# Optimization experiments

Measured on AMD Instinct MI355X. Metric: run time of the kernel, lower is better.

The kernel has to match this reference:

```python
import jax, jax.numpy as jnp
import numpy as np

LSTM = 400   # lstm_size
M = 20       # output_mixture_components
K = 10       # attention_mixture_components
A = 73       # alphabet_size


def setup_inputs() -> dict:
    key = jax.random.key(0)
    ks = jax.random.split(key, 24)
    B, T, U = 128, 800, 64

    def p(k, shape, scale=0.05):
        return jax.random.normal(k, shape, dtype=jnp.float32) * scale

    in1 = 3 + A                 # lstm1 input: [window, x]
    in2 = 3 + LSTM + A          # lstm2 input: [x, h1, window]
    in3 = 3 + 2 * LSTM + A      # lstm3 input: [x, h1, h2, window]

    inp = {
        "inputs": jax.random.normal(ks[0], (B, T, 3), dtype=jnp.float32) * 0.1,
        "char_seq": jax.random.randint(ks[1], (B, U), 0, A),
        "char_seq_lengths": jax.random.randint(ks[2], (B,), U // 2, U + 1),
        "bias": jnp.full((B,), 0.5, dtype=jnp.float32),
        # LSTMCell params (torch layout: gates order i,f,g,o)
        "Wih1": p(ks[3], (4 * LSTM, in1)), "Whh1": p(ks[4], (4 * LSTM, LSTM)),
        "bih1": p(ks[5], (4 * LSTM,)),    "bhh1": p(ks[6], (4 * LSTM,)),
        "Wih2": p(ks[7], (4 * LSTM, in2)), "Whh2": p(ks[8], (4 * LSTM, LSTM)),
        "bih2": p(ks[9], (4 * LSTM,)),    "bhh2": p(ks[10], (4 * LSTM,)),
        "Wih3": p(ks[11], (4 * LSTM, in3)), "Whh3": p(ks[12], (4 * LSTM, LSTM)),
        "bih3": p(ks[13], (4 * LSTM,)),    "bhh3": p(ks[14], (4 * LSTM,)),
        # Attention: h1 -> (alpha_hat, beta_hat, kappa_hat), 3K outputs
        "Wa": p(ks[15], (3 * K, LSTM)), "ba": p(ks[16], (3 * K,)),
        # GMM head: [h1,h2,h3] -> 6M+1 params
        "Wg": p(ks[17], (6 * M + 1, 3 * LSTM)), "bg": p(ks[18], (6 * M + 1,)),
    }
    return inp


def _lstm_cell(x, h, c, Wih, Whh, bih, bhh):
    gates = x @ Wih.T + bih + h @ Whh.T + bhh
    i, f, g, o = jnp.split(gates, 4, axis=-1)
    c = jax.nn.sigmoid(f) * c + jax.nn.sigmoid(i) * jnp.tanh(g)
    h = jax.nn.sigmoid(o) * jnp.tanh(c)
    return h, c


def reference(inputs, char_seq, char_seq_lengths, bias,
              Wih1, Whh1, bih1, bhh1,
              Wih2, Whh2, bih2, bhh2,
              Wih3, Whh3, bih3, bhh3,
              Wa, ba, Wg, bg):
    B, T, _ = inputs.shape
    U = char_seq.shape[1]
    oh = jax.nn.one_hot(char_seq, A, dtype=jnp.float32)            # [B,U,A]
    u = jnp.arange(U, dtype=jnp.float32)                            # [U]
    umask = (u[None, :] < char_seq_lengths[:, None].astype(jnp.float32)).astype(jnp.float32)
    bias_c = bias[:, None]

    def step(carry, x_t):
        h1, c1, h2, c2, h3, c3, window, kappa = carry
        h1, c1 = _lstm_cell(jnp.concatenate([window, x_t], 1), h1, c1, Wih1, Whh1, bih1, bhh1)
        # Gaussian-mixture attention window (Graves 2013)
        ap = h1 @ Wa.T + ba                                         # [B,3K]
        alpha_h, beta_h, kappa_h = jnp.split(ap, 3, axis=1)
        alpha = jnp.exp(alpha_h)
        beta = jnp.exp(beta_h)
        kappa = kappa + jnp.exp(kappa_h)                            # [B,K]
        # phi[b,u] = sum_k alpha exp(-beta (kappa-u)^2)
        g = jnp.exp(-beta[:, :, None] * (kappa[:, :, None] - u) ** 2)  # [B,K,U]
        phi = jnp.einsum('bk,bku->bu', alpha, g) * umask
        window = jnp.einsum('bu,bua->ba', phi, oh)                  # [B,A]
        h2, c2 = _lstm_cell(jnp.concatenate([x_t, h1, window], 1), h2, c2, Wih2, Whh2, bih2, bhh2)
        h3, c3 = _lstm_cell(jnp.concatenate([x_t, h1, h2, window], 1), h3, c3, Wih3, Whh3, bih3, bhh3)
        # GMM output layer with sampling bias
        out = jnp.concatenate([h1, h2, h3], 1) @ Wg.T + bg          # [B,6M+1]
        pi_hat = out[:, :M]
        mus = out[:, M:3 * M]
        sig_hat = out[:, 3 * M:5 * M]
        rho_hat = out[:, 5 * M:6 * M]
        e_hat = out[:, 6 * M:]
        pis = jax.nn.softmax(pi_hat * (1.0 + bias_c), axis=-1)
        sigmas = jnp.exp(sig_hat - bias_c)
        rhos = jnp.tanh(rho_hat)
        es = jax.nn.sigmoid(e_hat)
        return (h1, c1, h2, c2, h3, c3, window, kappa), (pis, sigmas, rhos, mus, es)

    z = lambda d: jnp.zeros((B, d), dtype=jnp.float32)
    carry0 = (z(LSTM), z(LSTM), z(LSTM), z(LSTM), z(LSTM), z(LSTM), z(A), z(K))
    _, outs = jax.lax.scan(step, carry0, jnp.swapaxes(inputs, 0, 1))
    pis, sigmas, rhos, mus, es = (jnp.swapaxes(o, 0, 1) for o in outs)  # [B,T,*]
    return pis, sigmas, rhos, mus, es
```

## Files before the change

### kernel.cpp

```cpp
#include <hip/hip_runtime.h>
#include <stdint.h>

typedef short s8v __attribute__((ext_vector_type(8)));
typedef _Float16 h8v __attribute__((ext_vector_type(8)));
typedef float f4v __attribute__((ext_vector_type(4)));
typedef unsigned short u16;
typedef unsigned int u32;
typedef unsigned long long u64;

#define TT 800
#define BB 128
#define UU 64
#define ALP 73
#define DD 400

#define G_BATCH 32
#define N_CLUS 4
#define N_MEM 50
#define NTHREADS 256

#define CX0 0
#define CX1 32
#define CWIN 64
#define CWINLO 160
#define CH1 256
#define CH2 672
#define CH3 1088
#define ACT_STRIDE 3072

#define NC1 17
#define NC2 30
#define NC3 43
#define NCO 39
#define NCA 13
#define F1 5
#define F2 8
#define F3 11
#define FA 4
#define FO 10

#define ACT_BYTES (32*ACT_STRIDE)
#define H1LO_OFF ACT_BYTES
#define H1LO_STRIDE 896
#define RBUF_OFF (H1LO_OFF + 32*H1LO_STRIDE)
#define ABK_OFF (RBUF_OFF + 16384)
#define WINS_OFF (ABK_OFF + 3840)
#define CHAR_OFF (RBUF_OFF + 32768)
#define LENS_OFF (CHAR_OFF + 2048)
#define BIASC_OFF (LENS_OFF + 128)
#define BCI_OFF (BIASC_OFF + 128)
#define BAS_OFF (BCI_OFF + 384)
#define BGS_OFF (BAS_OFF + 128)
#define LDS_TOTAL (BGS_OFF + 128)

#define OFF_SIG ((size_t)BB*TT*20)
#define OFF_RHO ((size_t)BB*TT*60)
#define OFF_MU  ((size_t)BB*TT*80)
#define OFF_ES  ((size_t)BB*TT*120)

#define HBUF_U32 25600

#define MFMA16(A,B,C) __builtin_amdgcn_mfma_f32_16x16x32_f16(__builtin_bit_cast(h8v,(A)),__builtin_bit_cast(h8v,(B)),(C),0,0,0)

#define AST(p,v) __hip_atomic_store((p),(v),__ATOMIC_RELAXED,__HIP_MEMORY_SCOPE_AGENT)
#define ALD(p)   __hip_atomic_load((p),__ATOMIC_RELAXED,__HIP_MEMORY_SCOPE_AGENT)

__device__ __forceinline__ u16 f16b(float x) {
  _Float16 h = (_Float16)x;
  return __builtin_bit_cast(u16, h);
}
__device__ __forceinline__ float f2f(u16 h) {
  return (float)__builtin_bit_cast(_Float16, h);
}
__device__ __forceinline__ float sigm(float x) { return 1.f / (1.f + __expf(-x)); }
__device__ __forceinline__ float tanhe(float x) {
  float e = __expf(-2.f * fabsf(x));
  float r = (1.f - e) / (1.f + e);
  return (x < 0.f) ? -r : r;
}
__device__ __forceinline__ int imin(int a, int b) { return a < b ? a : b; }
__device__ __forceinline__ int lstm_row(int mem, int n, int r) {
  return (n*2 + (r>>3))*400 + mem*8 + (r&7);
}
__device__ __forceinline__ int out_orow(int rc) {
  if (rc < 20) return rc;
  if (rc < 60) return 60 + (rc-20);
  if (rc < 80) return 100 + (rc-60);
  if (rc < 120) return 20 + (rc-80);
  if (rc == 120) return 120;
  return -1;
}
__device__ __forceinline__ s8v gath(const float* W, int ld, int grow, int cb, int valid, int k0) {
  union { s8v v; u16 u[8]; } r;
  #pragma unroll
  for (int j = 0; j < 8; ++j) {
    int k = k0 + j;
    float x = 0.f;
    if (grow >= 0 && k < valid) x = W[(size_t)grow * ld + cb + k];
    r.u[j] = f16b(x);
  }
  return r.v;
}
__device__ __forceinline__ s8v gathlo(const float* W, int ld, int grow, int cb, int valid, int k0) {
  union { s8v v; u16 u[8]; } r;
  #pragma unroll
  for (int j = 0; j < 8; ++j) {
    int k = k0 + j;
    float x = 0.f;
    if (grow >= 0 && k < valid) x = W[(size_t)grow * ld + cb + k];
    u16 hi = f16b(x);
    r.u[j] = f16b(x - f2f(hi));
  }
  return r.v;
}

extern "C" __global__ __launch_bounds__(NTHREADS, 1)
void hwrnn(const float* __restrict__ xin, const int* __restrict__ chq,
           const int* __restrict__ lenq, const float* __restrict__ biasq,
           const float* __restrict__ Wih1, const float* __restrict__ Whh1,
           const float* __restrict__ bih1, const float* __restrict__ bhh1,
           const float* __restrict__ Wih2, const float* __restrict__ Whh2,
           const float* __restrict__ bih2, const float* __restrict__ bhh2,
           const float* __restrict__ Wih3, const float* __restrict__ Whh3,
           const float* __restrict__ bih3, const float* __restrict__ bhh3,
           const float* __restrict__ Wa, const float* __restrict__ ba,
           const float* __restrict__ Wg, const float* __restrict__ bg,
           float* __restrict__ dout, u32* __restrict__ barr,
           u32* __restrict__ h1ring, u32* __restrict__ h2g, u32* __restrict__ h3g,
           u32* __restrict__ h1glo)
{
  extern __shared__ __align__(16) char sm[];
  const int tid = threadIdx.x;
  const int wv = tid >> 6;
  const int ln = tid & 63;
  const int cl = blockIdx.x & 3;
  const int mem = blockIdx.x >> 2;
  const int B0 = cl * G_BATCH;

  const int arow = ln & 15;
  const int k0 = (ln >> 4) * 8;
  const int ahi = (ln >> 4) * 16;
  const int axor = (ln & 7) << 4;
  const int rb0 = arow * ACT_STRIDE;
  const int rb1 = (16 + arow) * ACT_STRIDE;
  const int hb0 = H1LO_OFF + arow * H1LO_STRIDE;
  const int hb1 = H1LO_OFF + (16 + arow) * H1LO_STRIDE;
  const f4v az = {0.f, 0.f, 0.f, 0.f};

  for (int i = tid; i * 16 < RBUF_OFF; i += NTHREADS) *(f4v*)(sm + i*16) = az;
  for (int i = tid; i < 32*UU; i += NTHREADS) {
    int b = i >> 6, u = i & 63;
    ((unsigned char*)(sm + CHAR_OFF))[i] = (unsigned char)chq[(B0 + b)*UU + u];
  }
  if (tid < 32) {
    ((int*)(sm + LENS_OFF))[tid] = lenq[B0 + tid];
    ((float*)(sm + BIASC_OFF))[tid] = biasq[B0 + tid];
    ((float*)(sm + BAS_OFF))[tid] = (tid < 30) ? ba[tid] : 0.f;
    float v = 0.f;
    if (mem == 0) { int orow = out_orow(tid); if (orow >= 0) v = bg[orow]; }
    else if (mem >= 1 && mem <= 6 && tid < 16) {
      int orow = out_orow((mem+1)*16 + tid); if (orow >= 0) v = bg[orow];
    }
    ((float*)(sm + BGS_OFF))[tid] = v;
  }
  if (tid < 96) {
    int l = tid >> 5, r = tid & 31;
    int grow = lstm_row(mem, r >> 4, r & 15);
    const float* bi = (l == 0) ? bih1 : (l == 1) ? bih2 : bih3;
    const float* bh = (l == 0) ? bhh1 : (l == 1) ? bhh2 : bhh3;
    ((float*)(sm + BCI_OFF))[l*32 + r] = bi[grow] + bh[grow];
  }

  s8v wf1[F1][2], wf2[F2][2], wf3[F3][2], wfa[FA][2], walo[FA][2], wfo[2][FO];
  #pragma unroll
  for (int i = 0; i < F1; ++i) {
    int c = wv + 4*i;
    #pragma unroll
    for (int n = 0; n < 2; ++n) {
      s8v v = {0,0,0,0,0,0,0,0};
      if (c < NC1) {
        int grow = lstm_row(mem, n, arow);
        if (c == 0)      v = gath(Wih1, 76, grow, 73, 3, k0);
        else if (c <= 3) v = gath(Wih1, 76, grow, (c-1)*32, imin(32, 73-(c-1)*32), k0);
        else             v = gath(Whh1, 400, grow, (c-4)*32, imin(32, 400-(c-4)*32), k0);
      }
      wf1[i][n] = v;
    }
  }
  #pragma unroll
  for (int i = 0; i < F2; ++i) {
    int c = wv + 4*i;
    #pragma unroll
    for (int n = 0; n < 2; ++n) {
      s8v v = {0,0,0,0,0,0,0,0};
      if (c < NC2) {
        int grow = lstm_row(mem, n, arow);
        if (c == 0)       v = gath(Wih2, 476, grow, 0, 3, k0);
        else if (c <= 13) v = gath(Wih2, 476, grow, 3+32*(c-1), imin(32, 400-32*(c-1)), k0);
        else if (c <= 16) v = gath(Wih2, 476, grow, 403+32*(c-14), imin(32, 73-32*(c-14)), k0);
        else              v = gath(Whh2, 400, grow, 32*(c-17), imin(32, 400-32*(c-17)), k0);
      }
      wf2[i][n] = v;
    }
  }
  #pragma unroll
  for (int i = 0; i < F3; ++i) {
    int c = wv + 4*i;
    #pragma unroll
    for (int n = 0; n < 2; ++n) {
      s8v v = {0,0,0,0,0,0,0,0};
      if (c < NC3) {
        int grow = lstm_row(mem, n, arow);
        if (c == 0)       v = gath(Wih3, 876, grow, 0, 3, k0);
        else if (c <= 13) v = gath(Wih3, 876, grow, 3+32*(c-1), imin(32, 400-32*(c-1)), k0);
        else if (c <= 26) v = gath(Wih3, 876, grow, 403+32*(c-14), imin(32, 400-32*(c-14)), k0);
        else if (c <= 29) v = gath(Wih3, 876, grow, 803+32*(c-27), imin(32, 73-32*(c-27)), k0);
        else              v = gath(Whh3, 400, grow, 32*(c-30), imin(32, 400-32*(c-30)), k0);
      }
      wf3[i][n] = v;
    }
  }
  #pragma unroll
  for (int i = 0; i < FA; ++i) {
    int c = wv + 4*i;
    #pragma unroll
    for (int n = 0; n < 2; ++n) {
      s8v v = {0,0,0,0,0,0,0,0}, vl = v;
      if (c < NCA) {
        int rr = n*16 + arow;
        int grow = (rr < 30) ? rr : -1;
        v  = gath  (Wa, 400, grow, 32*c, imin(32, 400-32*c), k0);
        vl = gathlo(Wa, 400, grow, 32*c, imin(32, 400-32*c), k0);
      }
      wfa[i][n] = v; walo[i][n] = vl;
    }
  }
  #pragma unroll
  for (int o = 0; o < 2; ++o) {
    #pragma unroll
    for (int i = 0; i < FO; ++i) {
      s8v v = {0,0,0,0,0,0,0,0};
      int c = wv + 4*i;
      bool have = (mem == 0) || (mem >= 1 && mem <= 6 && o == 0);
      if (have && c < NCO) {
        int ct = (mem == 0) ? o : (mem + 1);
        int grow = out_orow(ct*16 + arow);
        if (c <= 12)      v = gath(Wg, 1200, grow, 32*c, imin(32, 400-32*c), k0);
        else if (c <= 25) v = gath(Wg, 1200, grow, 400+32*(c-13), imin(32, 400-32*(c-13)), k0);
        else              v = gath(Wg, 1200, grow, 800+32*(c-26), imin(32, 400-32*(c-26)), k0);
      }
      wfo[o][i] = v;
    }
  }

  auto LDA0 = [&](int cb2) -> s8v { return *(const s8v*)(sm + rb0 + ((cb2 + ahi) ^ axor)); };
  auto LDA1 = [&](int cb2) -> s8v { return *(const s8v*)(sm + rb1 + ((cb2 + ahi) ^ axor)); };
  auto LDL0 = [&](int cb2) -> s8v { return *(const s8v*)(sm + hb0 + ((cb2 + ahi) ^ axor)); };
  auto LDL1 = [&](int cb2) -> s8v { return *(const s8v*)(sm + hb1 + ((cb2 + ahi) ^ axor)); };
  auto WPART = [&](int slot, f4v a) {
    *(f4v*)(sm + RBUF_OFF + (((slot*4 + wv)*256) + (ln & 15)*16 + (ln >> 4)*4)*4) = a;
  };
  auto RBF = [&](int slot, int w, int col, int row) -> float {
    return ((float*)(sm + RBUF_OFF))[(slot*4 + w)*256 + col*16 + row];
  };
  auto RLD = [&](const u32* ring, int half) -> s8v {
    union { s8v v; u64 q[2]; } r;
    r.q[0] = ALD((const u64*)ring + ((size_t)(B0 + arow + 16*half)*DD + k0 >> 2));
    r.q[1] = ALD((const u64*)ring + ((size_t)(B0 + arow + 16*half)*DD + k0 + 4 >> 2));
    return r.v;
  };
  const int ub = tid >> 3, uu = tid & 7;
  auto LUPD = [&](int sb, int l, float& c, u32* hg, u32* hlo) {
    int mt = ub >> 4, rw = ub & 15;
    const float* bci = (const float*)(sm + BCI_OFF);
    float vi = bci[l*32 + uu], vf = bci[l*32 + 8 + uu];
    float vg = bci[l*32 + 16 + uu], vo = bci[l*32 + 24 + uu];
    #pragma unroll
    for (int w = 0; w < 4; ++w) {
      vi += RBF(sb + mt, w, uu, rw);
      vf += RBF(sb + mt, w, 8 + uu, rw);
      vg += RBF(sb + 2 + mt, w, uu, rw);
      vo += RBF(sb + 2 + mt, w, 8 + uu, rw);
    }
    c = sigm(vf)*c + sigm(vi)*tanhe(vg);
    float h = sigm(vo)*tanhe(c);
    u16 hb = f16b(h);
    float hl = h - f2f(hb);
    float ho = __shfl_xor(h, 1, 64);
    float hlo_o = __shfl_xor(hl, 1, 64);
    if (!(uu & 1)) {
      size_t gi = ((size_t)(B0 + ub)*DD + mem*8 + uu) >> 1;
      AST(hg + gi, (u32)hb | ((u32)f16b(ho) << 16));
      if (hlo) AST(hlo + gi, (u32)f16b(hl) | ((u32)f16b(hlo_o) << 16));
    }
  };
  auto STAGEH = [&](const u32* hg, int cbase) {
    u64 va[7], vb[7];
    #pragma unroll
    for (int s = 0; s < 7; ++s) {
      int idx = tid + s*NTHREADS;
      if (idx < 1600) {
        int b = idx / 50, c16 = idx % 50;
        const u64* p = (const u64*)(hg + (((size_t)(B0 + b)*DD + c16*8) >> 1));
        va[s] = ALD(p); vb[s] = ALD(p + 1);
      }
    }
    #pragma unroll
    for (int s = 0; s < 7; ++s) {
      int idx = tid + s*NTHREADS;
      if (idx < 1600) {
        int b = idx / 50, c16 = idx % 50;
        int off = b*ACT_STRIDE + ((2*(cbase + c16*8)) ^ ((b & 7) << 4));
        *(u64*)(sm + off) = va[s];
        *(u64*)(sm + off + 8) = vb[s];
      }
    }
  };
  auto STAGEHLO = [&](const u32* hg) {
    u64 va[7], vb[7];
    #pragma unroll
    for (int s = 0; s < 7; ++s) {
      int idx = tid + s*NTHREADS;
      if (idx < 1600) {
        int b = idx / 50, c16 = idx % 50;
        const u64* p = (const u64*)(hg + (((size_t)(B0 + b)*DD + c16*8) >> 1));
        va[s] = ALD(p); vb[s] = ALD(p + 1);
      }
    }
    #pragma unroll
    for (int s = 0; s < 7; ++s) {
      int idx = tid + s*NTHREADS;
      if (idx < 1600) {
        int b = idx / 50, c16 = idx % 50;
        int off = H1LO_OFF + b*H1LO_STRIDE + ((16*c16) ^ ((b & 7) << 4));
        *(u64*)(sm + off) = va[s];
        *(u64*)(sm + off + 8) = vb[s];
      }
    }
  };
  u32* cA = barr + cl*64;
  auto ARRIVE = [&](u32* ctr) {
    asm volatile("s_waitcnt vmcnt(0)" ::: "memory");
    __syncthreads();
    if (tid == 0) __hip_atomic_fetch_add(ctr, 1u, __ATOMIC_RELAXED, __HIP_MEMORY_SCOPE_AGENT);
  };
  auto WAITC = [&](u32* ctr, u32 tgt) {
    if (tid == 0) {
      while (ALD(ctr) < tgt) __builtin_amdgcn_s_sleep(1);
    }
    __syncthreads();
  };

  __syncthreads();
  if (tid < 96) {
    int b = tid/3, cc = tid%3;
    float x = xin[((size_t)(B0+b)*TT)*3 + cc];
    int off = b*ACT_STRIDE + ((2*(CX0 + cc)) ^ ((b&7)<<4));
    *(u16*)(sm + off) = f16b(x);
  }
  __syncthreads();

  float c1 = 0.f, c2 = 0.f, c3 = 0.f, kap0 = 0.f, kap1 = 0.f;

  for (int t = 0; t <= TT + 2; ++t) {
    const int pc = t & 1, pp = pc ^ 1;
    const int xc = pc ? CX1 : CX0;
    const int xp = pp ? CX1 : CX0;
    u32* ring_w = h1ring + (size_t)(t & 7) * HBUF_U32;

    if (t < TT) {
      f4v a1[4] = {az, az, az, az};
      #pragma unroll
      for (int i = 0; i < F1; ++i) {
        int c = wv + 4*i;
        if (c < NC1) {
          int cb = (c == 0) ? xc : (c <= 3) ? (CWIN + 32*(c-1)) : (CH1 + 32*(c-4));
          int cb2 = 2*cb;
          s8v x0 = LDA0(cb2), x1 = LDA1(cb2);
          a1[0] = MFMA16(x0, wf1[i][0], a1[0]);
          a1[1] = MFMA16(x1, wf1[i][0], a1[1]);
          a1[2] = MFMA16(x0, wf1[i][1], a1[2]);
          a1[3] = MFMA16(x1, wf1[i][1], a1[3]);
          if (c >= 1) {
            s8v l0, l1;
            if (c <= 3) { int lb2 = 2*(CWINLO + 32*(c-1)); l0 = LDA0(lb2); l1 = LDA1(lb2); }
            else        { int lb2 = 64*(c-4);              l0 = LDL0(lb2); l1 = LDL1(lb2); }
            a1[0] = MFMA16(l0, wf1[i][0], a1[0]);
            a1[1] = MFMA16(l1, wf1[i][0], a1[1]);
            a1[2] = MFMA16(l0, wf1[i][1], a1[2]);
            a1[3] = MFMA16(l1, wf1[i][1], a1[3]);
          }
        }
      }
      WPART(0, a1[0]); WPART(1, a1[1]); WPART(2, a1[2]); WPART(3, a1[3]);
    }
    __syncthreads();
    if (t < TT) LUPD(0, 0, c1, ring_w, h1glo + (size_t)pc * HBUF_U32);
    ARRIVE(cA);

    if (t >= 3 && mem <= 6) {
      const u32* r1 = h1ring + (size_t)((t + 5) & 7) * HBUF_U32;
      const u32* r2 = h2g   + (size_t)((t + 1) & 3) * HBUF_U32;
      const u32* r3 = h3g   + (size_t)((t + 1) & 3) * HBUF_U32;
      f4v ao[4] = {az, az, az, az};
      #pragma unroll
      for (int i = 0; i < FO; ++i) {
        int c = wv + 4*i;
        if (c < NCO) {
          const u32* rp = (c <= 12) ? (r1 + (size_t)c * 16)
                        : (c <= 25) ? (r2 + (size_t)(c - 13) * 16)
                        :             (r3 + (size_t)(c - 26) * 16);
          s8v x0 = RLD(rp, 0), x1 = RLD(rp, 1);
          ao[0] = MFMA16(x0, wfo[0][i], ao[0]);
          ao[1] = MFMA16(x1, wfo[0][i], ao[1]);
          if (mem == 0) {
            ao[2] = MFMA16(x0, wfo[1][i], ao[2]);
            ao[3] = MFMA16(x1, wfo[1][i], ao[3]);
          }
        }
      }
      WPART(4, ao[0]); WPART(5, ao[1]);
      if (mem == 0) { WPART(6, ao[2]); WPART(7, ao[3]); }
      __syncthreads();
      const float* bgs = (const float*)(sm + BGS_OFF);
      const float* bcv = (const float*)(sm + BIASC_OFF);
      int tt = t - 3;
      auto OSUM = [&](int rl, int b) -> float {
        int slot = 4 + ((mem == 0) ? ((rl >> 4)*2) : 0) + (b >> 4);
        float s = bgs[rl];
        #pragma unroll
        for (int w = 0; w < 4; ++w) s += RBF(slot, w, rl & 15, b & 15);
        return s;
      };
      if (mem == 0) {
        if (tid < 32) {
          int b = tid;
          float sc = 1.f + bcv[b];
          float pv[20]; float mx = -3e38f;
          #pragma unroll
          for (int r = 0; r < 20; ++r) { pv[r] = OSUM(r, b) * sc; mx = fmaxf(mx, pv[r]); }
          float den = 0.f;
          #pragma unroll
          for (int r = 0; r < 20; ++r) { pv[r] = __expf(pv[r] - mx); den += pv[r]; }
          float inv = 1.f / den;
          size_t ob = ((size_t)(B0 + b)*TT + tt);
          #pragma unroll
          for (int r = 0; r < 20; ++r) dout[ob*20 + r] = pv[r] * inv;
        }
        for (int idx = tid; idx < 12*32; idx += NTHREADS) {
          int rl = 20 + (idx >> 5), b = idx & 31;
          float v = OSUM(rl, b);
          size_t ob = ((size_t)(B0 + b)*TT + tt);
          dout[OFF_SIG + ob*40 + (rl - 20)] = __expf(v - bcv[b]);
        }
      } else {
        int RB = (mem + 1) * 16;
        for (int idx = tid; idx < 512; idx += NTHREADS) {
          int rl = idx >> 5, b = idx & 31;
          int rc = RB + rl;
          float v = OSUM(rl, b);
          size_t ob = ((size_t)(B0 + b)*TT + tt);
          if (rc < 60)        dout[OFF_SIG + ob*40 + (rc - 20)] = __expf(v - bcv[b]);
          else if (rc < 80)   dout[OFF_RHO + ob*20 + (rc - 60)] = tanhe(v);
          else if (rc < 120)  dout[OFF_MU  + ob*40 + (rc - 80)] = v;
          else if (rc == 120) dout[OFF_ES + ob] = sigm(v);
        }
      }
    }

    WAITC(cA, (u32)(t + 1) * N_MEM);

    if (t >= 2 && t <= TT) STAGEH(h3g + (size_t)((t + 2) & 3) * HBUF_U32, CH3);
    if (t >= 1 && t <= TT) STAGEH(h2g + (size_t)((t + 3) & 3) * HBUF_U32, CH2);
    __syncthreads();

    f4v a2[4] = {az, az, az, az};
    if (t >= 1 && t <= TT) {
      f4v a3[4] = {az, az, az, az};
      #pragma unroll
      for (int i = 0; i < F3; ++i) {
        int c = wv + 4*i;
        if (c < NC3) {
          int cb = (c == 0) ? xp
                 : (c <= 13) ? (CH1 + 32*(c-1))
                 : (c <= 26) ? (CH2 + 32*(c-14))
                 : (c <= 29) ? (CWIN + 32*(c-27))
                 : (CH3 + 32*(c-30));
          int cb2 = 2*cb;
          s8v x0 = LDA0(cb2), x1 = LDA1(cb2);
          a3[0] = MFMA16(x0, wf3[i][0], a3[0]);
          a3[1] = MFMA16(x1, wf3[i][0], a3[1]);
          a3[2] = MFMA16(x0, wf3[i][1], a3[2]);
          a3[3] = MFMA16(x1, wf3[i][1], a3[3]);
          if ((c >= 1 && c <= 13) || (c >= 27 && c <= 29)) {
            s8v l0, l1;
            if (c <= 13) { int lb2 = 64*(c-1);               l0 = LDL0(lb2); l1 = LDL1(lb2); }
            else         { int lb2 = 2*(CWINLO + 32*(c-27)); l0 = LDA0(lb2); l1 = LDA1(lb2); }
            a3[0] = MFMA16(l0, wf3[i][0], a3[0]);
            a3[1] = MFMA16(l1, wf3[i][0], a3[1]);
            a3[2] = MFMA16(l0, wf3[i][1], a3[2]);
            a3[3] = MFMA16(l1, wf3[i][1], a3[3]);
          }
        }
      }
      WPART(4, a3[0]); WPART(5, a3[1]); WPART(6, a3[2]); WPART(7, a3[3]);
    }
    if (t < TT) {
      #pragma unroll
      for (int i = 0; i < F2; ++i) {
        int c = wv + 4*i;
        if (c < NC2 && (c == 0 || c >= 17)) {
          int cb = (c == 0) ? xc : (CH2 + 32*(c-17));
          int cb2 = 2*cb;
          s8v x0 = LDA0(cb2), x1 = LDA1(cb2);
          a2[0] = MFMA16(x0, wf2[i][0], a2[0]);
          a2[1] = MFMA16(x1, wf2[i][0], a2[1]);
          a2[2] = MFMA16(x0, wf2[i][1], a2[2]);
          a2[3] = MFMA16(x1, wf2[i][1], a2[3]);
        }
      }
    }
    __syncthreads();

    if (t < TT) { STAGEH(ring_w, CH1); STAGEHLO(h1glo + (size_t)pc * HBUF_U32); }
    if (t + 1 < TT && tid < 96) {
      int b = tid/3, cc = tid%3;
      float x = xin[((size_t)(B0+b)*TT + (t+1))*3 + cc];
      int off = b*ACT_STRIDE + ((2*(xp + cc)) ^ ((b&7)<<4));
      *(u16*)(sm + off) = f16b(x);
    }
    __syncthreads();

    if (t < TT) {
      f4v aa[4] = {az, az, az, az};
      #pragma unroll
      for (int i = 0; i < FA; ++i) {
        int c = wv + 4*i;
        if (c < NCA) {
          int cb2 = 2*(CH1 + 32*c);
          int lb2 = 64*c;
          s8v x0 = LDA0(cb2), x1 = LDA1(cb2);
          s8v l0 = LDL0(lb2), l1 = LDL1(lb2);
          aa[0] = MFMA16(x0, wfa[i][0], aa[0]);
          aa[1] = MFMA16(x1, wfa[i][0], aa[1]);
          aa[2] = MFMA16(x0, wfa[i][1], aa[2]);
          aa[3] = MFMA16(x1, wfa[i][1], aa[3]);
          aa[0] = MFMA16(l0, wfa[i][0], aa[0]);
          aa[1] = MFMA16(l1, wfa[i][0], aa[1]);
          aa[2] = MFMA16(l0, wfa[i][1], aa[2]);
          aa[3] = MFMA16(l1, wfa[i][1], aa[3]);
          aa[0] = MFMA16(x0, walo[i][0], aa[0]);
          aa[1] = MFMA16(x1, walo[i][0], aa[1]);
          aa[2] = MFMA16(x0, walo[i][1], aa[2]);
          aa[3] = MFMA16(x1, walo[i][1], aa[3]);
        }
      }
      WPART(0, aa[0]); WPART(1, aa[1]); WPART(2, aa[2]); WPART(3, aa[3]);
    }
    if (t >= 1 && t <= TT) LUPD(4, 2, c3, h3g + (size_t)((t + 3) & 3) * HBUF_U32, nullptr);
    __syncthreads();

    if (t < TT) {
      float* wins = (float*)(sm + WINS_OFF);
      for (int i = tid; i < 32*80; i += NTHREADS) wins[i] = 0.f;
      float* abk = (float*)(sm + ABK_OFF);
      const float* bas = (const float*)(sm + BAS_OFF);
      #pragma unroll
      for (int half = 0; half < 2; ++half) {
        int idx = tid + half*NTHREADS;
        if (idx < 320) {
          int b = idx & 31, j = idx >> 5;
          float ah = bas[j], bh = bas[10+j], kh = bas[20+j];
          #pragma unroll
          for (int w = 0; w < 4; ++w) {
            ah += RBF(0 + (b>>4), w, j, b & 15);
            if (j < 6) bh += RBF(0 + (b>>4), w, 10 + j, b & 15);
            else       bh += RBF(2 + (b>>4), w, j - 6, b & 15);
            kh += RBF(2 + (b>>4), w, 4 + j, b & 15);
          }
          float& kp = half ? kap1 : kap0;
          kp += __expf(kh);
          abk[0*320 + b*10 + j] = __expf(ah);
          abk[1*320 + b*10 + j] = __expf(bh);
          abk[2*320 + b*10 + j] = kp;
        }
      }
      __syncthreads();

      const unsigned char* chs = (const unsigned char*)(sm + CHAR_OFF);
      const int* lns = (const int*)(sm + LENS_OFF);
      for (int idx = tid; idx < 32*64; idx += NTHREADS) {
        int b = idx >> 6, u = idx & 63;
        if (u < lns[b]) {
          float ph = 0.f, fu = (float)u;
          #pragma unroll
          for (int j = 0; j < 10; ++j) {
            float d = abk[2*320 + b*10 + j] - fu;
            ph += abk[0*320 + b*10 + j] * __expf(-abk[1*320 + b*10 + j]*d*d);
          }
          atomicAdd(&wins[b*80 + (int)chs[b*64 + u]], ph);
        }
      }
      __syncthreads();

      for (int idx = tid; idx < 32*96; idx += NTHREADS) {
        int b = idx / 96, cc = idx % 96;
        float v = (cc < ALP) ? wins[b*80 + cc] : 0.f;
        u16 hi = f16b(v);
        u16 lo = f16b(v - f2f(hi));
        int sw = (b&7) << 4;
        *(u16*)(sm + b*ACT_STRIDE + ((2*(CWIN + cc)) ^ sw)) = hi;
        *(u16*)(sm + b*ACT_STRIDE + ((2*(CWINLO + cc)) ^ sw)) = lo;
      }
      __syncthreads();

      #pragma unroll
      for (int i = 0; i < F2; ++i) {
        int c = wv + 4*i;
        if (c >= 1 && c <= 16) {
          int cb = (c <= 13) ? (CH1 + 32*(c-1)) : (CWIN + 32*(c-14));
          int cb2 = 2*cb;
          s8v x0 = LDA0(cb2), x1 = LDA1(cb2);
          a2[0] = MFMA16(x0, wf2[i][0], a2[0]);
          a2[1] = MFMA16(x1, wf2[i][0], a2[1]);
          a2[2] = MFMA16(x0, wf2[i][1], a2[2]);
          a2[3] = MFMA16(x1, wf2[i][1], a2[3]);
          s8v l0, l1;
          if (c <= 13) { int lb2 = 64*(c-1);               l0 = LDL0(lb2); l1 = LDL1(lb2); }
          else         { int lb2 = 2*(CWINLO + 32*(c-14)); l0 = LDA0(lb2); l1 = LDA1(lb2); }
          a2[0] = MFMA16(l0, wf2[i][0], a2[0]);
          a2[1] = MFMA16(l1, wf2[i][0], a2[1]);
          a2[2] = MFMA16(l0, wf2[i][1], a2[2]);
          a2[3] = MFMA16(l1, wf2[i][1], a2[3]);
        }
      }
      WPART(0, a2[0]); WPART(1, a2[1]); WPART(2, a2[2]); WPART(3, a2[3]);
      __syncthreads();

      LUPD(0, 1, c2, h2g + (size_t)(t & 3) * HBUF_U32, nullptr);
    }
  }
}

extern "C" void kernel_launch(void* const* d_in, const int* in_sizes, int n_in,
                              void* d_out, int out_size, void* d_ws, size_t ws_size,
                              hipStream_t stream) {
  (void)in_sizes; (void)n_in; (void)out_size; (void)ws_size;
  const float* xin  = (const float*)d_in[0];
  const int*   chq  = (const int*)d_in[1];
  const int*   lnq  = (const int*)d_in[2];
  const float* bq   = (const float*)d_in[3];
  const float* Wih1 = (const float*)d_in[4];
  const float* Whh1 = (const float*)d_in[5];
  const float* bih1 = (const float*)d_in[6];
  const float* bhh1 = (const float*)d_in[7];
  const float* Wih2 = (const float*)d_in[8];
  const float* Whh2 = (const float*)d_in[9];
  const float* bih2 = (const float*)d_in[10];
  const float* bhh2 = (const float*)d_in[11];
  const float* Wih3 = (const float*)d_in[12];
  const float* Whh3 = (const float*)d_in[13];
  const float* bih3 = (const float*)d_in[14];
  const float* bhh3 = (const float*)d_in[15];
  const float* Wa   = (const float*)d_in[16];
  const float* ba   = (const float*)d_in[17];
  const float* Wg   = (const float*)d_in[18];
  const float* bg   = (const float*)d_in[19];
  float* dout = (float*)d_out;
  char* ws = (char*)d_ws;
  u32* barr   = (u32*)ws;
  u32* h1ring = (u32*)(ws + 4096);
  u32* h2g    = (u32*)(ws + 4096 + 819200);
  u32* h3g    = (u32*)(ws + 4096 + 1232896 - 4096);
  u32* h1glo  = (u32*)(ws + 1642496);

  hipMemsetAsync(ws, 0, 4096, stream);
  hipFuncSetAttribute(reinterpret_cast<const void*>(hwrnn),
                      hipFuncAttributeMaxDynamicSharedMemorySize, LDS_TOTAL);
  hipLaunchKernelGGL(hwrnn, dim3(N_CLUS * N_MEM), dim3(NTHREADS), LDS_TOTAL, stream,
                     xin, chq, lnq, bq, Wih1, Whh1, bih1, bhh1, Wih2, Whh2, bih2, bhh2,
                     Wih3, Whh3, bih3, bhh3, Wa, ba, Wg, bg, dout, barr,
                     h1ring, h2g, h3g, h1glo);
}
```

Before: 17.96 ms.

## Replace atomic counter barrier with per-block flag slots and swizzle reduction buffer

The cluster barrier changes from one shared atomic counter, which each of the 50 member blocks incremented, to a per-block flag slot holding the step number. A 64-lane wavefront polls all 50 slots in parallel and uses __all to decide when every block has arrived. This removes contention on the atomic counter. The LDS partial-sum buffer layout is also XOR-swizzled to reduce bank conflicts, and the GMM output loads are hoisted ahead of their MFMAs to overlap memory latency. The workspace offsets grow to make room for the padded slots.

```diff
diff --git a/kernel.cpp b/kernel.cpp
--- a/kernel.cpp
+++ b/kernel.cpp
@@ -89,6 +89,9 @@
   if (rc < 120) return 20 + (rc-80);
   if (rc == 120) return 120;
   return -1;
+}
+__device__ __forceinline__ int rbswz(int col, int row) {
+  return col*16 + ((((row >> 2) ^ ((col >> 1) & 3)) << 2) | (row & 3));
 }
 __device__ __forceinline__ s8v gath(const float* W, int ld, int grow, int cb, int valid, int k0) {
   union { s8v v; u16 u[8]; } r;
@@ -258,10 +261,12 @@
   auto LDL0 = [&](int cb2) -> s8v { return *(const s8v*)(sm + hb0 + ((cb2 + ahi) ^ axor)); };
   auto LDL1 = [&](int cb2) -> s8v { return *(const s8v*)(sm + hb1 + ((cb2 + ahi) ^ axor)); };
   auto WPART = [&](int slot, f4v a) {
-    *(f4v*)(sm + RBUF_OFF + (((slot*4 + wv)*256) + (ln & 15)*16 + (ln >> 4)*4)*4) = a;
+    int col = ln & 15;
+    int q = (ln >> 4) ^ ((col >> 1) & 3);
+    *(f4v*)(sm + RBUF_OFF + (((slot*4 + wv)*256) + col*16 + q*4)*4) = a;
   };
   auto RBF = [&](int slot, int w, int col, int row) -> float {
-    return ((float*)(sm + RBUF_OFF))[(slot*4 + w)*256 + col*16 + row];
+    return ((float*)(sm + RBUF_OFF))[(slot*4 + w)*256 + rbswz(col, row)];
   };
   auto RLD = [&](const u32* ring, int half) -> s8v {
     union { s8v v; u64 q[2]; } r;
@@ -338,15 +343,19 @@
       }
     }
   };
-  u32* cA = barr + cl*64;
-  auto ARRIVE = [&](u32* ctr) {
+  u32* slots = barr + cl * (N_MEM * 16);
+  auto ARRIVE = [&](u32 step) {
     asm volatile("s_waitcnt vmcnt(0)" ::: "memory");
     __syncthreads();
-    if (tid == 0) __hip_atomic_fetch_add(ctr, 1u, __ATOMIC_RELAXED, __HIP_MEMORY_SCOPE_AGENT);
+    if (tid == 0) AST(slots + mem * 16, step);
   };
-  auto WAITC = [&](u32* ctr, u32 tgt) {
-    if (tid == 0) {
-      while (ALD(ctr) < tgt) __builtin_amdgcn_s_sleep(1);
+  auto WAITC = [&](u32 tgt) {
+    if (tid < 64) {
+      for (;;) {
+        u32 v = (ln < N_MEM) ? ALD(slots + ln * 16) : tgt;
+        if (__all((int)(v >= tgt))) break;
+        __builtin_amdgcn_s_sleep(1);
+      }
     }
     __syncthreads();
   };
@@ -396,13 +405,13 @@
     }
     __syncthreads();
     if (t < TT) LUPD(0, 0, c1, ring_w, h1glo + (size_t)pc * HBUF_U32);
-    ARRIVE(cA);
+    ARRIVE((u32)(t + 1));
 
     if (t >= 3 && mem <= 6) {
       const u32* r1 = h1ring + (size_t)((t + 5) & 7) * HBUF_U32;
       const u32* r2 = h2g   + (size_t)((t + 1) & 3) * HBUF_U32;
       const u32* r3 = h3g   + (size_t)((t + 1) & 3) * HBUF_U32;
-      f4v ao[4] = {az, az, az, az};
+      s8v xf0[FO], xf1[FO];
       #pragma unroll
       for (int i = 0; i < FO; ++i) {
         int c = wv + 4*i;
@@ -410,12 +419,19 @@
           const u32* rp = (c <= 12) ? (r1 + (size_t)c * 16)
                         : (c <= 25) ? (r2 + (size_t)(c - 13) * 16)
                         :             (r3 + (size_t)(c - 26) * 16);
-          s8v x0 = RLD(rp, 0), x1 = RLD(rp, 1);
-          ao[0] = MFMA16(x0, wfo[0][i], ao[0]);
-          ao[1] = MFMA16(x1, wfo[0][i], ao[1]);
+          xf0[i] = RLD(rp, 0); xf1[i] = RLD(rp, 1);
+        }
+      }
+      f4v ao[4] = {az, az, az, az};
+      #pragma unroll
+      for (int i = 0; i < FO; ++i) {
+        int c = wv + 4*i;
+        if (c < NCO) {
+          ao[0] = MFMA16(xf0[i], wfo[0][i], ao[0]);
+          ao[1] = MFMA16(xf1[i], wfo[0][i], ao[1]);
           if (mem == 0) {
-            ao[2] = MFMA16(x0, wfo[1][i], ao[2]);
-            ao[3] = MFMA16(x1, wfo[1][i], ao[3]);
+            ao[2] = MFMA16(xf0[i], wfo[1][i], ao[2]);
+            ao[3] = MFMA16(xf1[i], wfo[1][i], ao[3]);
           }
         }
       }
@@ -468,7 +484,7 @@
       }
     }
 
-    WAITC(cA, (u32)(t + 1) * N_MEM);
+    WAITC((u32)(t + 1));
 
     if (t >= 2 && t <= TT) STAGEH(h3g + (size_t)((t + 2) & 3) * HBUF_U32, CH3);
     if (t >= 1 && t <= TT) STAGEH(h2g + (size_t)((t + 3) & 3) * HBUF_U32, CH2);
@@ -669,12 +685,12 @@
   float* dout = (float*)d_out;
   char* ws = (char*)d_ws;
   u32* barr   = (u32*)ws;
-  u32* h1ring = (u32*)(ws + 4096);
-  u32* h2g    = (u32*)(ws + 4096 + 819200);
-  u32* h3g    = (u32*)(ws + 4096 + 1232896 - 4096);
-  u32* h1glo  = (u32*)(ws + 1642496);
-
-  hipMemsetAsync(ws, 0, 4096, stream);
+  u32* h1ring = (u32*)(ws + 16384);
+  u32* h2g    = (u32*)(ws + 16384 + 819200);
+  u32* h3g    = (u32*)(ws + 16384 + 1228800);
+  u32* h1glo  = (u32*)(ws + 16384 + 1638400);
+
+  hipMemsetAsync(ws, 0, 16384, stream);
   hipFuncSetAttribute(reinterpret_cast<const void*>(hwrnn),
                       hipFuncAttributeMaxDynamicSharedMemorySize, LDS_TOTAL);
   hipLaunchKernelGGL(hwrnn, dim3(N_CLUS * N_MEM), dim3(NTHREADS), LDS_TOTAL, stream,
```

Measured after the change: 21.90 ms. +21.9%, slower.
